# Kernel optimization log

Hardware: AMD Instinct MI355X
Metric: run time of the kernel (lower is better)

The kernel has to match this reference:

```python
import jax, jax.numpy as jnp
import numpy as np


def setup_inputs() -> dict:
    key = jax.random.key(0)
    k1, k2, k3 = jax.random.split(key, 3)
    bs, nvars, T, input_dim = 8, 16, 512, 256
    embed_dim, num_embed, codebook_num = 128, 512, 4
    inp = jax.random.normal(k1, (bs, nvars, T, input_dim), dtype=jnp.float32)
    # xavier_normal_ for (input_dim, embed_dim): std = sqrt(2/(fan_in+fan_out))
    xavier_std = float(np.sqrt(2.0 / (input_dim + embed_dim)))
    projector = jax.random.normal(k2, (input_dim, embed_dim), dtype=jnp.float32) * xavier_std
    codebook = jax.random.normal(k3, (codebook_num, num_embed, embed_dim), dtype=jnp.float32)
    return {"input": inp, "projector": projector, "codebook": codebook}


def reference(input, projector, codebook):
    # project: [b,n,t,input_dim] @ [input_dim,embed_dim] -> [b,n,t,d]
    x = jnp.matmul(input, projector)
    # L2-normalize along last dim (matches torch .norm(dim=-1,keepdim=True) division)
    x = x / jnp.linalg.norm(x, axis=-1, keepdims=True)
    cb = codebook / jnp.linalg.norm(codebook, axis=-1, keepdims=True)
    # cosine similarity: [b,n,t,c,m]
    similarity = jnp.einsum('bntd,cmd->bntcm', x, cb)
    # nearest code per codebook: [b,n,t,c]
    idx = jnp.argmax(similarity, axis=-1)
    return idx
```

## Files before the change

kernel.cpp:

```cpp
#include <hip/hip_runtime.h>
#include <math.h>

#define DIN    256
#define DEMB   128
#define NCB    4
#define MCODES 512
#define NCODE  2048
#define MARGIN 1.5e-4f

using bf16x8 = __attribute__((ext_vector_type(8))) short;
using f32x16 = __attribute__((ext_vector_type(16))) float;

static __device__ __forceinline__ unsigned short f2bf(float f) {
    unsigned u = __float_as_uint(f);
    u += 0x7FFFu + ((u >> 16) & 1u);
    return (unsigned short)(u >> 16);
}
static __device__ __forceinline__ float bf2f(unsigned short h) {
    return __uint_as_float(((unsigned)h) << 16);
}
static __device__ __forceinline__ float4 ld4(const float* p) {
    return *reinterpret_cast<const float4*>(p);
}
static __device__ __forceinline__ void gload_lds16(const void* g, void* l) {
    __builtin_amdgcn_global_load_lds(
        (const __attribute__((address_space(1))) void*)g,
        (__attribute__((address_space(3))) void*)l, 16, 0, 0);
}

__global__ __launch_bounds__(256) void prep_codebook(
        const float* __restrict__ cb, float* __restrict__ cbn,
        unsigned short* __restrict__ cbA) {
    const int w = threadIdx.x >> 6, lane = threadIdx.x & 63;
    const int code = blockIdx.x * 4 + w;
    const float2 v = reinterpret_cast<const float2*>(cb + (size_t)code * DEMB)[lane];
    float ss = v.x * v.x + v.y * v.y;
#pragma unroll
    for (int m = 1; m < 64; m <<= 1) ss += __shfl_xor(ss, m, 64);
    const float rn = 1.0f / sqrtf(ss);
    const float x0 = v.x * rn, x1 = v.y * rn;
    reinterpret_cast<float2*>(cbn + (size_t)code * DEMB)[lane] = make_float2(x0, x1);

    const unsigned short h0 = f2bf(x0), h1 = f2bf(x1);
    const unsigned short l0 = f2bf(x0 - bf2f(h0)), l1 = f2bf(x1 - bf2f(h1));
    const int ct = code >> 5, ci = code & 31;
    const int kt = lane >> 3, g = (lane >> 2) & 1, i = 2 * (lane & 3);
    const size_t base = ((size_t)ct * 1024 + kt * 128 + g * 32 + ci) * 8 + i;
    *reinterpret_cast<ushort2*>(cbA + base)       = make_ushort2(h0, h1);
    *reinterpret_cast<ushort2*>(cbA + base + 512) = make_ushort2(l0, l1);
}

__global__ __launch_bounds__(256) void prep_proj(
        const float* __restrict__ proj, unsigned short* __restrict__ pjA) {
    const int t = blockIdx.x * 256 + threadIdx.x;
    const int ci = t & 31, g = (t >> 5) & 1, kt = (t >> 6) & 15, mt = t >> 10;
    const int m = mt * 32 + ci;
    const size_t base = ((size_t)(mt * 16 + kt) * 3) * 512 + (size_t)(g * 32 + ci) * 8;
#pragma unroll
    for (int i = 0; i < 8; ++i) {
        const float v = proj[(size_t)(kt * 16 + g * 8 + i) * DEMB + m];
        const unsigned short h = f2bf(v);
        const float r1 = v - bf2f(h);
        const unsigned short md = f2bf(r1);
        const float r2 = r1 - bf2f(md);
        pjA[base + i]        = h;
        pjA[base + 512 + i]  = md;
        pjA[base + 1024 + i] = f2bf(r2);
    }
}

__global__ __launch_bounds__(256) void project_mfma(
        const float* __restrict__ inp, const unsigned short* __restrict__ pjA,
        float* __restrict__ xw, float* __restrict__ rnw) {
    __shared__ __align__(16) short sA[3][6144];
    const int tid = threadIdx.x;
    const int lane = tid & 63, wv = tid >> 6, kg = lane >> 5;
    const int row = blockIdx.x * 128 + wv * 32 + (lane & 31);
    const float* xr = inp + (size_t)row * DIN;

    auto stageA = [&](int buf, int kt) {
#pragma unroll
        for (int c = 0; c < 3; ++c) {
            const unsigned short* g =
                pjA + ((size_t)(wv * 16 + kt) * 3 + c) * 512 + (size_t)lane * 8;
            gload_lds16(g, &sA[buf][(wv * 3 + c) * 512]);
        }
    };
    auto ldin = [&](float4& a, float4& b, int kt) {
        a = ld4(xr + kt * 16 + kg * 8);
        b = ld4(xr + kt * 16 + kg * 8 + 4);
    };
    auto split8 = [&](const float4& a, const float4& b,
                      bf16x8& H, bf16x8& M, bf16x8& L) {
        const float xs[8] = {a.x, a.y, a.z, a.w, b.x, b.y, b.z, b.w};
#pragma unroll
        for (int e = 0; e < 8; ++e) {
            const float v = xs[e];
            const unsigned short h = f2bf(v);
            const float r1 = v - bf2f(h);
            const unsigned short md = f2bf(r1);
            const float r2 = r1 - bf2f(md);
            H[e] = (short)h; M[e] = (short)md; L[e] = (short)f2bf(r2);
        }
    };

    f32x16 accP[4], accQ[4];
#pragma unroll
    for (int mt = 0; mt < 4; ++mt)
#pragma unroll
        for (int r = 0; r < 16; ++r) { accP[mt][r] = 0.0f; accQ[mt][r] = 0.0f; }

    float4 nA0, nA1, nB0, nB1;
    stageA(0, 0);
    ldin(nA0, nA1, 0);
    stageA(1, 1);

#pragma unroll
    for (int kt = 0; kt < 16; ++kt) {
        if (kt < 15) asm volatile("s_waitcnt vmcnt(3)" ::: "memory");
        else         asm volatile("s_waitcnt vmcnt(0)" ::: "memory");
        __builtin_amdgcn_s_barrier();
        asm volatile("" ::: "memory");

        const float4 c0 = (kt & 1) ? nB0 : nA0;
        const float4 c1 = (kt & 1) ? nB1 : nA1;
        if (kt < 15) {
            if (kt & 1) ldin(nA0, nA1, kt + 1);
            else        ldin(nB0, nB1, kt + 1);
        }
        if (kt + 2 < 16) stageA((kt + 2) % 3, kt + 2);

        bf16x8 Bh, Bm, Bl;
        split8(c0, c1, Bh, Bm, Bl);
        const int bc = kt % 3;
#pragma unroll
        for (int mt = 0; mt < 4; ++mt) {
            const bf16x8 Ah = *reinterpret_cast<const bf16x8*>(&sA[bc][(mt * 3 + 0) * 512 + lane * 8]);
            const bf16x8 Am = *reinterpret_cast<const bf16x8*>(&sA[bc][(mt * 3 + 1) * 512 + lane * 8]);
            const bf16x8 Al = *reinterpret_cast<const bf16x8*>(&sA[bc][(mt * 3 + 2) * 512 + lane * 8]);
            accP[mt] = __builtin_amdgcn_mfma_f32_32x32x16_bf16(Ah, Bh, accP[mt], 0, 0, 0);
            accQ[mt] = __builtin_amdgcn_mfma_f32_32x32x16_bf16(Ah, Bm, accQ[mt], 0, 0, 0);
            accQ[mt] = __builtin_amdgcn_mfma_f32_32x32x16_bf16(Am, Bh, accQ[mt], 0, 0, 0);
            accQ[mt] = __builtin_amdgcn_mfma_f32_32x32x16_bf16(Ah, Bl, accQ[mt], 0, 0, 0);
            accQ[mt] = __builtin_amdgcn_mfma_f32_32x32x16_bf16(Al, Bh, accQ[mt], 0, 0, 0);
            accQ[mt] = __builtin_amdgcn_mfma_f32_32x32x16_bf16(Am, Bm, accQ[mt], 0, 0, 0);
        }
    }

    float ss = 0.0f;
#pragma unroll
    for (int mt = 0; mt < 4; ++mt)
#pragma unroll
        for (int q = 0; q < 4; ++q) {
            float4 v;
            v.x = accP[mt][q * 4 + 0] + accQ[mt][q * 4 + 0];
            v.y = accP[mt][q * 4 + 1] + accQ[mt][q * 4 + 1];
            v.z = accP[mt][q * 4 + 2] + accQ[mt][q * 4 + 2];
            v.w = accP[mt][q * 4 + 3] + accQ[mt][q * 4 + 3];
            ss += v.x * v.x + v.y * v.y + v.z * v.z + v.w * v.w;
            *reinterpret_cast<float4*>(xw + (size_t)row * DEMB + mt * 32 + q * 8 + kg * 4) = v;
        }
    ss += __shfl_xor(ss, 32, 64);
    if (lane < 32) rnw[row] = 1.0f / sqrtf(ss);
}

__global__ __launch_bounds__(256) void project_kernel(
        const float* __restrict__ inp, const float* __restrict__ proj,
        float* __restrict__ xw, float* __restrict__ rnw) {
    const int tid = threadIdx.x, tx = tid & 31, ty = tid >> 5;
    const int rowBase = blockIdx.x * 64;

    float acc1[8][4];
#pragma unroll
    for (int i = 0; i < 8; ++i)
#pragma unroll
        for (int j = 0; j < 4; ++j) acc1[i][j] = 0.0f;

    const float* inRow0 = inp + (size_t)(rowBase + ty) * DIN;
    const float* pjCol  = proj + tx * 4;

    float4 ivA[8], ivB[8], pjA[4], pjB[4];
    auto load_step = [&](float4 iv[8], float4 pj[4], int kk) {
#pragma unroll
        for (int j = 0; j < 4; ++j) pj[j] = ld4(pjCol + (size_t)(kk + j) * DEMB);
#pragma unroll
        for (int i = 0; i < 8; ++i) iv[i] = ld4(inRow0 + (size_t)(8 * i) * DIN + kk);
    };
    auto fma_step = [&](const float4 iv[8], const float4 pj[4]) {
#pragma unroll
        for (int i = 0; i < 8; ++i) {
            const float* ivp = reinterpret_cast<const float*>(&iv[i]);
#pragma unroll
            for (int j = 0; j < 4; ++j) {
                acc1[i][0] = fmaf(ivp[j], pj[j].x, acc1[i][0]);
                acc1[i][1] = fmaf(ivp[j], pj[j].y, acc1[i][1]);
                acc1[i][2] = fmaf(ivp[j], pj[j].z, acc1[i][2]);
                acc1[i][3] = fmaf(ivp[j], pj[j].w, acc1[i][3]);
            }
        }
    };
    load_step(ivA, pjA, 0);
#pragma unroll 1
    for (int k = 0; k < DIN; k += 8) {
        load_step(ivB, pjB, k + 4);
        fma_step(ivA, pjA);
        if (k + 8 < DIN) load_step(ivA, pjA, k + 8);
        fma_step(ivB, pjB);
    }
#pragma unroll
    for (int i = 0; i < 8; ++i) {
        const int r = rowBase + ty + 8 * i;
        float ss = acc1[i][0] * acc1[i][0] + acc1[i][1] * acc1[i][1] +
                   acc1[i][2] * acc1[i][2] + acc1[i][3] * acc1[i][3];
#pragma unroll
        for (int mm = 1; mm < 32; mm <<= 1) ss += __shfl_xor(ss, mm, 64);
        if (tx == 0) rnw[r] = 1.0f / sqrtf(ss);
        *reinterpret_cast<float4*>(xw + (size_t)r * DEMB + tx * 4) =
            make_float4(acc1[i][0], acc1[i][1], acc1[i][2], acc1[i][3]);
    }
}

__global__ __launch_bounds__(512) void sim_kernel(
        const float* __restrict__ xw, const float* __restrict__ rnw,
        const unsigned short* __restrict__ cbA,
        int* __restrict__ out, int* __restrict__ unc_cnt,
        int* __restrict__ unc_list) {
    __shared__ __align__(16) short sA[3][8192];
    const int tid = threadIdx.x;
    const int lane = tid & 63, wv = tid >> 6;
    const int kg = lane >> 5;
    const int cbi = blockIdx.x & 3;
    const int rowBase = (blockIdx.x >> 2) * 256;
    const int row = rowBase + wv * 32 + (lane & 31);

    const short* gA = (const short*)cbA + (size_t)cbi * 16 * 8192;

    auto stage = [&](int buf, int t) {
        const short* g = gA + (size_t)t * 8192 + wv * 1024 + lane * 8;
        short* l = &sA[buf][wv * 1024];
#pragma unroll
        for (int c = 0; c < 2; ++c)
            gload_lds16(g + c * 512, l + c * 512);
    };

    stage(0, 0);
    stage(1, 1);

    bf16x8 Bhi[8], Blo[8];
    {
        const float rn = rnw[row];
        const float* xr = xw + (size_t)row * DEMB;
#pragma unroll
        for (int kt = 0; kt < 8; ++kt) {
            const float4 f0 = ld4(xr + kt * 16 + kg * 8);
            const float4 f1 = ld4(xr + kt * 16 + kg * 8 + 4);
            const float xs[8] = {f0.x, f0.y, f0.z, f0.w, f1.x, f1.y, f1.z, f1.w};
            bf16x8 hv, lv;
#pragma unroll
            for (int e = 0; e < 8; ++e) {
                const float xn = xs[e] * rn;
                const unsigned short h = f2bf(xn);
                hv[e] = (short)h;
                lv[e] = (short)f2bf(xn - bf2f(h));
            }
            Bhi[kt] = hv; Blo[kt] = lv;
        }
    }

    float t1 = -INFINITY, t2 = -INFINITY; int i1 = 0;

#pragma unroll 1
    for (int ct = 0; ct < 16; ++ct) {
        if (ct < 15) asm volatile("s_waitcnt vmcnt(2)" ::: "memory");
        else         asm volatile("s_waitcnt vmcnt(0)" ::: "memory");
        __builtin_amdgcn_s_barrier();
        asm volatile("" ::: "memory");
        if (ct + 2 < 16) stage((ct + 2) % 3, ct + 2);

        f32x16 accA, accB1, accB2;
#pragma unroll
        for (int r = 0; r < 16; ++r) { accA[r] = 0.0f; accB1[r] = 0.0f; accB2[r] = 0.0f; }
        const short* pa = &sA[ct % 3][lane * 8];
#pragma unroll
        for (int kt = 0; kt < 8; ++kt) {
            const bf16x8 Ahi = *reinterpret_cast<const bf16x8*>(pa + kt * 1024);
            const bf16x8 Alo = *reinterpret_cast<const bf16x8*>(pa + kt * 1024 + 512);
            accA  = __builtin_amdgcn_mfma_f32_32x32x16_bf16(Ahi, Bhi[kt], accA,  0, 0, 0);
            accB1 = __builtin_amdgcn_mfma_f32_32x32x16_bf16(Ahi, Blo[kt], accB1, 0, 0, 0);
            accB2 = __builtin_amdgcn_mfma_f32_32x32x16_bf16(Alo, Bhi[kt], accB2, 0, 0, 0);
        }
#pragma unroll
        for (int r = 0; r < 16; ++r) {
            const float v = (accA[r] + accB1[r]) + accB2[r];
            const int gidx = ct * 32 + ((r & 3) + 8 * (r >> 2) + 4 * kg);
            t2 = fmaxf(t2, fminf(v, t1));
            if (v > t1) { t1 = v; i1 = gidx; }
        }
    }

    const float o1 = __shfl_xor(t1, 32, 64);
    const float o2 = __shfl_xor(t2, 32, 64);
    const int   oi = __shfl_xor(i1, 32, 64);
    const float m2 = fmaxf(fmaxf(t2, o2), fminf(t1, o1));
    if (o1 > t1 || (o1 == t1 && oi < i1)) { t1 = o1; i1 = oi; }
    const bool unc = (t1 - m2) < MARGIN;
    if (lane < 32 && !unc)
        out[(size_t)row * NCB + cbi] = i1;

    unsigned long long msk = __ballot(unc && lane < 32);
    if (lane == 0 && msk) {
        const int n = __popcll(msk);
        int base = atomicAdd(unc_cnt, n);
        while (msk) {
            const int r = __ffsll(msk) - 1; msk &= msk - 1;
            unc_list[base++] = ((rowBase + wv * 32 + r) << 2) | cbi;
        }
    }
}

__global__ __launch_bounds__(256) void recheck_kernel(
        const float* __restrict__ inp, const float* __restrict__ proj,
        const float* __restrict__ cbn,
        const int* __restrict__ unc_cnt, const int* __restrict__ unc_list,
        int* __restrict__ out) {
    __shared__ float sx[4][DEMB];
    const int lane = threadIdx.x & 63, wv = threadIdx.x >> 6;
    const int n = *unc_cnt;
    for (int it = blockIdx.x * 4 + wv; it < n; it += gridDim.x * 4) {
        const int item = unc_list[it];
        const int row = item >> 2, cbi = item & 3;
        {
            const float* ir = inp + (size_t)row * DIN;
            float a0 = 0.0f, a1 = 0.0f;
#pragma unroll 1
            for (int k = 0; k < DIN; k += 4) {
                const float4 iv = ld4(ir + k);
                const float* ivp = reinterpret_cast<const float*>(&iv);
#pragma unroll
                for (int j = 0; j < 4; ++j) {
                    a0 = fmaf(ivp[j], proj[(size_t)(k + j) * DEMB + lane],      a0);
                    a1 = fmaf(ivp[j], proj[(size_t)(k + j) * DEMB + lane + 64], a1);
                }
            }
            sx[wv][lane] = a0; sx[wv][lane + 64] = a1;
        }
        float best = -INFINITY; int bi = 0;
#pragma unroll 1
        for (int j = 0; j < 8; ++j) {
            const int c = lane + 64 * j;
            const float* cv = cbn + ((size_t)cbi * MCODES + c) * DEMB;
            float s0 = 0, s1 = 0, s2 = 0, s3 = 0;
#pragma unroll
            for (int k = 0; k < DEMB; k += 4) {
                const float4 xk = ld4(&sx[wv][k]);
                const float4 ck = ld4(cv + k);
                s0 = fmaf(xk.x, ck.x, s0); s1 = fmaf(xk.y, ck.y, s1);
                s2 = fmaf(xk.z, ck.z, s2); s3 = fmaf(xk.w, ck.w, s3);
            }
            const float s = (s0 + s1) + (s2 + s3);
            if (s > best) { best = s; bi = c; }
        }
#pragma unroll
        for (int mm = 1; mm < 64; mm <<= 1) {
            const float ov = __shfl_xor(best, mm, 64);
            const int   oc = __shfl_xor(bi, mm, 64);
            if (ov > best || (ov == best && oc < bi)) { best = ov; bi = oc; }
        }
        if (lane == 0) out[(size_t)row * NCB + cbi] = bi;
    }
}

__global__ __launch_bounds__(256) void fused_quantize_kernel(
        const float* __restrict__ inp, const float* __restrict__ proj,
        const float* __restrict__ cbn, const unsigned short* __restrict__ cbA,
        int* __restrict__ out) {
    __shared__ float sX[128][132];
    __shared__ float sRn[128];
    const int tid = threadIdx.x;
    const int tx = tid & 31, ty = tid >> 5;
    const int rowBase = blockIdx.x * 128;

#pragma unroll 1
    for (int p = 0; p < 2; ++p) {
        float acc1[8][4];
#pragma unroll
        for (int i = 0; i < 8; ++i)
#pragma unroll
            for (int j = 0; j < 4; ++j) acc1[i][j] = 0.0f;
        const float* inRow0 = inp + (size_t)(rowBase + p * 64 + ty) * DIN;
        const float* pjCol  = proj + tx * 4;
        float4 ivA[8], ivB[8], pjA[4], pjB[4];
        auto load_step = [&](float4 iv[8], float4 pj[4], int kk) {
#pragma unroll
            for (int j = 0; j < 4; ++j) pj[j] = ld4(pjCol + (size_t)(kk + j) * DEMB);
#pragma unroll
            for (int i = 0; i < 8; ++i) iv[i] = ld4(inRow0 + (size_t)(8 * i) * DIN + kk);
        };
        auto fma_step = [&](const float4 iv[8], const float4 pj[4]) {
#pragma unroll
            for (int i = 0; i < 8; ++i) {
                const float* ivp = reinterpret_cast<const float*>(&iv[i]);
#pragma unroll
                for (int j = 0; j < 4; ++j) {
                    acc1[i][0] = fmaf(ivp[j], pj[j].x, acc1[i][0]);
                    acc1[i][1] = fmaf(ivp[j], pj[j].y, acc1[i][1]);
                    acc1[i][2] = fmaf(ivp[j], pj[j].z, acc1[i][2]);
                    acc1[i][3] = fmaf(ivp[j], pj[j].w, acc1[i][3]);
                }
            }
        };
        load_step(ivA, pjA, 0);
#pragma unroll 1
        for (int k = 0; k < DIN; k += 8) {
            load_step(ivB, pjB, k + 4);
            fma_step(ivA, pjA);
            if (k + 8 < DIN) load_step(ivA, pjA, k + 8);
            fma_step(ivB, pjB);
        }
#pragma unroll
        for (int i = 0; i < 8; ++i) {
            const int r = p * 64 + ty + 8 * i;
            float ss = acc1[i][0] * acc1[i][0] + acc1[i][1] * acc1[i][1] +
                       acc1[i][2] * acc1[i][2] + acc1[i][3] * acc1[i][3];
#pragma unroll
            for (int mm = 1; mm < 32; mm <<= 1) ss += __shfl_xor(ss, mm, 64);
            if (tx == 0) sRn[r] = 1.0f / sqrtf(ss);
            *reinterpret_cast<float4*>(&sX[r][tx * 4]) =
                make_float4(acc1[i][0], acc1[i][1], acc1[i][2], acc1[i][3]);
        }
    }
    __syncthreads();

    const int lane = tid & 63, wv = tid >> 6;
    const int kg = lane >> 5;
    const int rowL = wv * 32 + (lane & 31);
    bf16x8 Bhi[8], Blo[8];
    {
        const float rn = sRn[rowL];
#pragma unroll
        for (int kt = 0; kt < 8; ++kt) {
            const int k0 = kt * 16 + kg * 8;
            float4 f0 = ld4(&sX[rowL][k0]);
            float4 f1 = ld4(&sX[rowL][k0 + 4]);
            float xs[8] = {f0.x, f0.y, f0.z, f0.w, f1.x, f1.y, f1.z, f1.w};
            bf16x8 hv, lv;
#pragma unroll
            for (int e = 0; e < 8; ++e) {
                const float xn = xs[e] * rn;
                const unsigned short h = f2bf(xn);
                hv[e] = (short)h;
                lv[e] = (short)f2bf(xn - bf2f(h));
            }
            Bhi[kt] = hv; Blo[kt] = lv;
        }
    }
    float t1 = -INFINITY, t2 = -INFINITY; int i1 = 0;
    const short* pA = reinterpret_cast<const short*>(cbA) + (size_t)lane * 8;
#pragma unroll 1
    for (int ct = 0; ct < 64; ++ct) {
        if ((ct & 1) == 0) __syncthreads();
        const short* pct = pA + (size_t)ct * 8192;
        f32x16 accA, accB;
#pragma unroll
        for (int r = 0; r < 16; ++r) { accA[r] = 0.0f; accB[r] = 0.0f; }
#pragma unroll
        for (int kt = 0; kt < 8; ++kt) {
            const bf16x8 Ahi = *reinterpret_cast<const bf16x8*>(pct + kt * 1024);
            const bf16x8 Alo = *reinterpret_cast<const bf16x8*>(pct + kt * 1024 + 512);
            accA = __builtin_amdgcn_mfma_f32_32x32x16_bf16(Ahi, Bhi[kt], accA, 0, 0, 0);
            accB = __builtin_amdgcn_mfma_f32_32x32x16_bf16(Ahi, Blo[kt], accB, 0, 0, 0);
            accB = __builtin_amdgcn_mfma_f32_32x32x16_bf16(Alo, Bhi[kt], accB, 0, 0, 0);
        }
#pragma unroll
        for (int r = 0; r < 16; ++r) {
            const float v = accA[r] + accB[r];
            const int gidx = ct * 32 + ((r & 3) + 8 * (r >> 2) + 4 * kg);
            t2 = fmaxf(t2, fminf(v, t1));
            if (v > t1) { t1 = v; i1 = gidx; }
        }
        if ((ct & 15) == 15) {
            const int cbi = ct >> 4;
            const float o1 = __shfl_xor(t1, 32, 64);
            const float o2 = __shfl_xor(t2, 32, 64);
            const int   oi = __shfl_xor(i1, 32, 64);
            const float m2 = fmaxf(fmaxf(t2, o2), fminf(t1, o1));
            if (o1 > t1 || (o1 == t1 && oi < i1)) { t1 = o1; i1 = oi; }
            const bool unc = (t1 - m2) < MARGIN;
            if (lane < 32 && !unc)
                out[(size_t)(rowBase + rowL) * NCB + cbi] = i1 - cbi * MCODES;
            unsigned long long msk = __ballot(unc && lane < 32);
            while (msk) {
                const int r = __ffsll(msk) - 1; msk &= msk - 1;
                const int rl = wv * 32 + r;
                float best = -INFINITY; int bi = 0;
#pragma unroll 1
                for (int j = 0; j < 8; ++j) {
                    const int c = lane + 64 * j;
                    const float* cv = cbn + ((size_t)cbi * MCODES + c) * DEMB;
                    float s0 = 0, s1 = 0, s2 = 0, s3 = 0;
#pragma unroll
                    for (int k = 0; k < DEMB; k += 4) {
                        const float4 xk = ld4(&sX[rl][k]);
                        const float4 ck = ld4(cv + k);
                        s0 = fmaf(xk.x, ck.x, s0); s1 = fmaf(xk.y, ck.y, s1);
                        s2 = fmaf(xk.z, ck.z, s2); s3 = fmaf(xk.w, ck.w, s3);
                    }
                    const float s = (s0 + s1) + (s2 + s3);
                    if (s > best) { best = s; bi = c; }
                }
#pragma unroll
                for (int mm = 1; mm < 64; mm <<= 1) {
                    const float ov = __shfl_xor(best, mm, 64);
                    const int   oc = __shfl_xor(bi, mm, 64);
                    if (ov > best || (ov == best && oc < bi)) { best = ov; bi = oc; }
                }
                if (lane == 0) out[(size_t)(rowBase + rl) * NCB + cbi] = bi;
            }
            t1 = -INFINITY; t2 = -INFINITY; i1 = 0;
        }
    }
}

extern "C" void kernel_launch(void* const* d_in, const int* in_sizes, int n_in,
                              void* d_out, int out_size, void* d_ws, size_t ws_size,
                              hipStream_t stream) {
    const float* inp  = (const float*)d_in[0];
    const float* proj = (const float*)d_in[1];
    const float* cb   = (const float*)d_in[2];
    int* out = (int*)d_out;

    char* ws = (char*)d_ws;
    float* cbn = (float*)ws;
    unsigned short* cbA = (unsigned short*)(ws + (1 << 20));
    float* rnw = (float*)(ws + (2 << 20));
    float* xw  = (float*)(ws + (2 << 20) + (1 << 18));
    const size_t off_cnt = (size_t)(2 << 20) + (1 << 18) + ((size_t)32 << 20);
    int* unc_cnt  = (int*)(ws + off_cnt);
    int* unc_list = (int*)(ws + off_cnt + 256);
    const size_t off_pjA = off_cnt + 256 + (1 << 20);
    unsigned short* pjA = (unsigned short*)(ws + off_pjA);
    const size_t need_old = off_pjA;
    const size_t need_new = off_pjA + 192 * 1024;

    hipLaunchKernelGGL(prep_codebook, dim3(NCODE / 4), dim3(256), 0, stream,
                       cb, cbn, cbA);
    if (ws_size >= need_old) {
        hipMemsetAsync(unc_cnt, 0, 4, stream);
        if (ws_size >= need_new) {
            hipLaunchKernelGGL(prep_proj, dim3(16), dim3(256), 0, stream, proj, pjA);
            hipLaunchKernelGGL(project_mfma, dim3(512), dim3(256), 0, stream,
                               inp, pjA, xw, rnw);
        } else {
            hipLaunchKernelGGL(project_kernel, dim3(1024), dim3(256), 0, stream,
                               inp, proj, xw, rnw);
        }
        hipLaunchKernelGGL(sim_kernel, dim3(256 * NCB), dim3(512), 0, stream,
                           xw, rnw, cbA, out, unc_cnt, unc_list);
        hipLaunchKernelGGL(recheck_kernel, dim3(512), dim3(256), 0, stream,
                           inp, proj, cbn, unc_cnt, unc_list, out);
    } else {
        hipLaunchKernelGGL(fused_quantize_kernel, dim3(512), dim3(256), 0, stream,
                           inp, proj, cbn, cbA, out);
    }
}
```

Before: 231.3 us.

## Restructure sim kernel: all codebooks per block, software-pipelined argmax with packed keys

The similarity kernel now runs 512 blocks of 256 threads, each covering 128 rows across all four codebooks, so the projected rows converted to bf16 hi/lo in registers are reused four times instead of once. The epilogue of each code tile is deferred one iteration so it can overlap the next tile's MFMAs, and s_setprio is raised around the MFMA section. The running top-2 tracking uses unsigned keys that pack the index into the low mantissa bits, which turns the comparisons into branchless integer max/min. Because truncating those bits loses precision, the uncertainty margin is widened, which may send more items to the recheck kernel.

Result: slower. 264.8 us (+14.5%).

```diff
diff --git a/kernel.cpp b/kernel.cpp
--- a/kernel.cpp
+++ b/kernel.cpp
@@ -6,7 +6,7 @@
 #define NCB    4
 #define MCODES 512
 #define NCODE  2048
-#define MARGIN 1.5e-4f
+#define MARGIN 2.5e-4f
 
 using bf16x8 = __attribute__((ext_vector_type(8))) short;
 using f32x16 = __attribute__((ext_vector_type(16))) float;
@@ -22,6 +22,8 @@
 static __device__ __forceinline__ float4 ld4(const float* p) {
     return *reinterpret_cast<const float4*>(p);
 }
+static __device__ __forceinline__ unsigned umaxu(unsigned a, unsigned b) { return a > b ? a : b; }
+static __device__ __forceinline__ unsigned uminu(unsigned a, unsigned b) { return a < b ? a : b; }
 static __device__ __forceinline__ void gload_lds16(const void* g, void* l) {
     __builtin_amdgcn_global_load_lds(
         (const __attribute__((address_space(1))) void*)g,
@@ -220,7 +222,7 @@
     }
 }
 
-__global__ __launch_bounds__(512) void sim_kernel(
+__global__ __launch_bounds__(256) void sim_kernel(
         const float* __restrict__ xw, const float* __restrict__ rnw,
         const unsigned short* __restrict__ cbA,
         int* __restrict__ out, int* __restrict__ unc_cnt,
@@ -229,17 +231,14 @@
     const int tid = threadIdx.x;
     const int lane = tid & 63, wv = tid >> 6;
     const int kg = lane >> 5;
-    const int cbi = blockIdx.x & 3;
-    const int rowBase = (blockIdx.x >> 2) * 256;
+    const int rowBase = blockIdx.x * 128;
     const int row = rowBase + wv * 32 + (lane & 31);
 
-    const short* gA = (const short*)cbA + (size_t)cbi * 16 * 8192;
-
     auto stage = [&](int buf, int t) {
-        const short* g = gA + (size_t)t * 8192 + wv * 1024 + lane * 8;
-        short* l = &sA[buf][wv * 1024];
-#pragma unroll
-        for (int c = 0; c < 2; ++c)
+        const short* g = (const short*)cbA + (size_t)t * 8192 + wv * 2048 + lane * 8;
+        short* l = &sA[buf][wv * 2048];
+#pragma unroll
+        for (int c = 0; c < 4; ++c)
             gload_lds16(g + c * 512, l + c * 512);
     };
 
@@ -267,55 +266,85 @@
         }
     }
 
-    float t1 = -INFINITY, t2 = -INFINITY; int i1 = 0;
-
-#pragma unroll 1
-    for (int ct = 0; ct < 16; ++ct) {
-        if (ct < 15) asm volatile("s_waitcnt vmcnt(2)" ::: "memory");
-        else         asm volatile("s_waitcnt vmcnt(0)" ::: "memory");
+    f32x16 TWO, ZERO;
+#pragma unroll
+    for (int r = 0; r < 16; ++r) { TWO[r] = 2.0f; ZERO[r] = 0.0f; }
+
+    f32x16 accA, accB1, accB2;
+    unsigned t1k = 0u, t2k = 0u;
+
+    auto epilogue = [&](int gprev) {
+        const f32x16 v = (accA + accB1) + accB2;
+        const unsigned base255 = 255u - ((unsigned)(gprev & 15) << 4);
+#pragma unroll
+        for (int r = 0; r < 16; ++r) {
+            const unsigned kb = (__float_as_uint(v[r]) & 0xFFFFFF00u) | (base255 - r);
+            t2k = umaxu(t2k, uminu(kb, t1k));
+            t1k = umaxu(t1k, kb);
+        }
+    };
+    auto finalize = [&](int cb) {
+        const unsigned o1 = (unsigned)__shfl_xor((int)t1k, 32, 64);
+        const unsigned o2 = (unsigned)__shfl_xor((int)t2k, 32, 64);
+        const unsigned m2 = umaxu(umaxu(t2k, o2), uminu(t1k, o1));
+        const unsigned w1 = umaxu(t1k, o1);
+        const int wkg = (o1 > t1k) ? (kg ^ 1) : ((o1 == t1k) ? 0 : kg);
+        const float gap = __uint_as_float(w1 & 0xFFFFFF00u) -
+                          __uint_as_float(m2 & 0xFFFFFF00u);
+        const bool unc = gap < MARGIN;
+        const unsigned rank8 = 255u - (w1 & 0xFFu);
+        const int ctl = (int)(rank8 >> 4), rr = (int)(rank8 & 15u);
+        const int code = ctl * 32 + (rr & 3) + 8 * (rr >> 2) + 4 * wkg;
+        if (lane < 32 && !unc)
+            out[(size_t)row * NCB + cb] = code;
+        unsigned long long msk = __ballot(unc && lane < 32);
+        if (lane == 0 && msk) {
+            const int n = __popcll(msk);
+            int base = atomicAdd(unc_cnt, n);
+            while (msk) {
+                const int r = __ffsll(msk) - 1; msk &= msk - 1;
+                unc_list[base++] = ((rowBase + wv * 32 + r) << 2) | cb;
+            }
+        }
+        t1k = 0u; t2k = 0u;
+    };
+
+#pragma unroll 1
+    for (int g = 0; g < 64; ++g) {
+        if (g < 63) asm volatile("s_waitcnt vmcnt(4)" ::: "memory");
+        else        asm volatile("s_waitcnt vmcnt(0)" ::: "memory");
         __builtin_amdgcn_s_barrier();
         asm volatile("" ::: "memory");
-        if (ct + 2 < 16) stage((ct + 2) % 3, ct + 2);
-
-        f32x16 accA, accB1, accB2;
-#pragma unroll
-        for (int r = 0; r < 16; ++r) { accA[r] = 0.0f; accB1[r] = 0.0f; accB2[r] = 0.0f; }
-        const short* pa = &sA[ct % 3][lane * 8];
+        if (g + 2 < 64) stage((g + 2) % 3, g + 2);
+
+        const short* pa = &sA[g % 3][lane * 8];
+
+        f32x16 pA = accA, pB1 = accB1, pB2 = accB2;
+        __builtin_amdgcn_s_setprio(1);
 #pragma unroll
         for (int kt = 0; kt < 8; ++kt) {
             const bf16x8 Ahi = *reinterpret_cast<const bf16x8*>(pa + kt * 1024);
             const bf16x8 Alo = *reinterpret_cast<const bf16x8*>(pa + kt * 1024 + 512);
-            accA  = __builtin_amdgcn_mfma_f32_32x32x16_bf16(Ahi, Bhi[kt], accA,  0, 0, 0);
-            accB1 = __builtin_amdgcn_mfma_f32_32x32x16_bf16(Ahi, Blo[kt], accB1, 0, 0, 0);
-            accB2 = __builtin_amdgcn_mfma_f32_32x32x16_bf16(Alo, Bhi[kt], accB2, 0, 0, 0);
-        }
-#pragma unroll
-        for (int r = 0; r < 16; ++r) {
-            const float v = (accA[r] + accB1[r]) + accB2[r];
-            const int gidx = ct * 32 + ((r & 3) + 8 * (r >> 2) + 4 * kg);
-            t2 = fmaxf(t2, fminf(v, t1));
-            if (v > t1) { t1 = v; i1 = gidx; }
-        }
-    }
-
-    const float o1 = __shfl_xor(t1, 32, 64);
-    const float o2 = __shfl_xor(t2, 32, 64);
-    const int   oi = __shfl_xor(i1, 32, 64);
-    const float m2 = fmaxf(fmaxf(t2, o2), fminf(t1, o1));
-    if (o1 > t1 || (o1 == t1 && oi < i1)) { t1 = o1; i1 = oi; }
-    const bool unc = (t1 - m2) < MARGIN;
-    if (lane < 32 && !unc)
-        out[(size_t)row * NCB + cbi] = i1;
-
-    unsigned long long msk = __ballot(unc && lane < 32);
-    if (lane == 0 && msk) {
-        const int n = __popcll(msk);
-        int base = atomicAdd(unc_cnt, n);
-        while (msk) {
-            const int r = __ffsll(msk) - 1; msk &= msk - 1;
-            unc_list[base++] = ((rowBase + wv * 32 + r) << 2) | cbi;
-        }
-    }
+            accA  = __builtin_amdgcn_mfma_f32_32x32x16_bf16(Ahi, Bhi[kt], kt ? accA  : TWO,  0, 0, 0);
+            accB1 = __builtin_amdgcn_mfma_f32_32x32x16_bf16(Ahi, Blo[kt], kt ? accB1 : ZERO, 0, 0, 0);
+            accB2 = __builtin_amdgcn_mfma_f32_32x32x16_bf16(Alo, Bhi[kt], kt ? accB2 : ZERO, 0, 0, 0);
+        }
+        __builtin_amdgcn_s_setprio(0);
+
+        if (g > 0) {
+            const f32x16 v = (pA + pB1) + pB2;
+            const unsigned base255 = 255u - ((unsigned)((g - 1) & 15) << 4);
+#pragma unroll
+            for (int r = 0; r < 16; ++r) {
+                const unsigned kb = (__float_as_uint(v[r]) & 0xFFFFFF00u) | (base255 - r);
+                t2k = umaxu(t2k, uminu(kb, t1k));
+                t1k = umaxu(t1k, kb);
+            }
+            if ((g & 15) == 0) finalize((g >> 4) - 1);
+        }
+    }
+    epilogue(63);
+    finalize(3);
 }
 
 __global__ __launch_bounds__(256) void recheck_kernel(
@@ -554,7 +583,7 @@
             hipLaunchKernelGGL(project_kernel, dim3(1024), dim3(256), 0, stream,
                                inp, proj, xw, rnw);
         }
-        hipLaunchKernelGGL(sim_kernel, dim3(256 * NCB), dim3(512), 0, stream,
+        hipLaunchKernelGGL(sim_kernel, dim3(512), dim3(256), 0, stream,
                            xw, rnw, cbA, out, unc_cnt, unc_list);
         hipLaunchKernelGGL(recheck_kernel, dim3(512), dim3(256), 0, stream,
                            inp, proj, cbn, unc_cnt, unc_list, out);
```
